# Kernel optimization log

Hardware: AMD Instinct MI355X
Metric: run time of the kernel (lower is better)

Reference implementation:

```python
import jax, jax.numpy as jnp
import numpy as np

B, S = 64, 256
VOCAB, DL, DA, DV = 30522, 300, 74, 35
DH, GH, LH, RH = 128, 64, 128, 128  # modality dim, proj-GRU hidden, LSTM hidden, RGN hidden


def _gru_dir(x, Wi, Wh, bi, bh):
    # x: [B,S,D] -> [B,S,H]; torch GRU gate order (r, z, n)
    xg = x @ Wi + bi  # [B,S,3H] precomputed input projections
    H = Wh.shape[0]
    def step(h, xg_t):
        hg = h @ Wh + bh
        xr, xz, xn = jnp.split(xg_t, 3, axis=-1)
        hr, hz, hn = jnp.split(hg, 3, axis=-1)
        r = jax.nn.sigmoid(xr + hr)
        z = jax.nn.sigmoid(xz + hz)
        n = jnp.tanh(xn + r * hn)
        h = (1.0 - z) * n + z * h
        return h, h
    h0 = jnp.zeros((x.shape[0], H), x.dtype)
    _, ys = jax.lax.scan(step, h0, jnp.swapaxes(xg, 0, 1))
    return jnp.swapaxes(ys, 0, 1)


def _bigru(x, Wi, Wh, bi, bh):
    f = _gru_dir(x, Wi[0], Wh[0], bi[0], bh[0])
    b = _gru_dir(x[:, ::-1], Wi[1], Wh[1], bi[1], bh[1])[:, ::-1]
    return jnp.concatenate([f, b], axis=-1)


def _lstm_dir(x, Wi, Wh, bi, bh):
    xg = x @ Wi + bi  # [B,S,4H]; torch LSTM gate order (i, f, g, o)
    H = Wh.shape[0]
    def step(carry, xg_t):
        h, c = carry
        g = xg_t + h @ Wh + bh
        i, f, gg, o = jnp.split(g, 4, axis=-1)
        c = jax.nn.sigmoid(f) * c + jax.nn.sigmoid(i) * jnp.tanh(gg)
        h = jax.nn.sigmoid(o) * jnp.tanh(c)
        return (h, c), h
    z = jnp.zeros((x.shape[0], H), x.dtype)
    _, ys = jax.lax.scan(step, (z, z), jnp.swapaxes(xg, 0, 1))
    return jnp.swapaxes(ys, 0, 1)


def _bilstm(x, Wi, Wh, bi, bh):
    f = _lstm_dir(x, Wi[0], Wh[0], bi[0], bh[0])
    b = _lstm_dir(x[:, ::-1], Wi[1], Wh[1], bi[1], bh[1])[:, ::-1]
    return jnp.concatenate([f, b], axis=-1)


def _rgn_scan(x, h0, Wx, Wh, b):
    # RGNCell: gated recurrent cell (GRU-style), returns final state [B,H]
    xg = x @ Wx + b  # [B,S,3H]
    def step(h, xg_t):
        hg = h @ Wh
        xr, xz, xn = jnp.split(xg_t, 3, axis=-1)
        hr, hz, hn = jnp.split(hg, 3, axis=-1)
        r = jax.nn.sigmoid(xr + hr)
        z = jax.nn.sigmoid(xz + hz)
        n = jnp.tanh(xn + r * hn)
        return (1.0 - z) * n + z * h, None
    h, _ = jax.lax.scan(step, h0, jnp.swapaxes(xg, 0, 1))
    return h


def _xattn(q, kv):
    # parameter-free scaled dot-product cross-modal attention (JCAF)
    scale = 1.0 / np.sqrt(q.shape[-1]).astype(np.float32)
    s = jnp.einsum('bsd,btd->bst', q, kv) * scale
    return jnp.einsum('bst,btd->bsd', jax.nn.softmax(s, axis=-1), kv)


def _forward(sentences, acoustic, video, state0, state1, emb,
             proj_l_W, proj_l_b, proj_a_W, proj_a_b, proj_v_W, proj_v_b,
             gru_Wi, gru_Wh, gru_bi, gru_bh,
             lstm_Wi, lstm_Wh, lstm_bi, lstm_bh,
             rgn_Wx, rgn_Wh, rgn_b, fc1_W, fc1_b, fc2_W, fc2_b):
    enc = emb[sentences]                          # LanguageEmbeddingLayer: [B,S,DL]
    # SeqEncoder: project each modality to 128-d (dropout off in eval)
    seq_l = enc @ proj_l_W + proj_l_b             # [B,S,128]
    seq_a = acoustic @ proj_a_W + proj_a_b
    seq_v = video @ proj_v_W + proj_v_b
    # project_l/a/v: bidirectional GRU 128 -> 2*64 = 128
    x_l = _bigru(seq_l, gru_Wi[0], gru_Wh[0], gru_bi[0], gru_bh[0])
    x_a = _bigru(seq_a, gru_Wi[1], gru_Wh[1], gru_bi[1], gru_bh[1])
    x_v = _bigru(seq_v, gru_Wi[2], gru_Wh[2], gru_bi[2], gru_bh[2])
    # JCAF: each modality enriched by cross-attention to the other two
    fin_txt = x_l + _xattn(x_l, x_a) + _xattn(x_l, x_v)
    fin_aud = x_a + _xattn(x_a, x_l) + _xattn(x_a, x_v)
    fin_vis = x_v + _xattn(x_v, x_l) + _xattn(x_v, x_a)
    tstep = jnp.concatenate([fin_txt, fin_aud, fin_vis], axis=-1)      # [B,S,384]
    step_fusion = _bilstm(tstep, lstm_Wi, lstm_Wh, lstm_bi, lstm_bh)   # [B,S,256]
    # two custom RGNCell recurrences: forward sweep + reversed sweep
    out0 = _rgn_scan(step_fusion, state0, rgn_Wx[0], rgn_Wh[0], rgn_b[0])
    out1 = _rgn_scan(step_fusion[:, ::-1], state1, rgn_Wx[1], rgn_Wh[1], rgn_b[1])
    h = jax.nn.leaky_relu((out0 + out1) @ fc1_W + fc1_b)
    return h @ fc2_W + fc2_b                     # [B,1]


def setup_inputs():
    keys = iter(jax.random.split(jax.random.key(0), 48))
    def rn(shape, s=0.05):
        return jax.random.normal(next(keys), shape, jnp.float32) * s
    return {
        'sentences': jax.random.randint(next(keys), (B, S), 0, VOCAB),
        'acoustic': jax.random.normal(next(keys), (B, S, DA), jnp.float32),
        'video': jax.random.normal(next(keys), (B, S, DV), jnp.float32),
        'state0': jax.random.normal(next(keys), (B, RH), jnp.float32),
        'state1': jax.random.normal(next(keys), (B, RH), jnp.float32),
        'emb': rn((VOCAB, DL), 0.1),
        'proj_l_W': rn((DL, DH)), 'proj_l_b': rn((DH,)),
        'proj_a_W': rn((DA, DH)), 'proj_a_b': rn((DH,)),
        'proj_v_W': rn((DV, DH)), 'proj_v_b': rn((DH,)),
        'gru_Wi': rn((3, 2, DH, 3 * GH)), 'gru_Wh': rn((3, 2, GH, 3 * GH)),
        'gru_bi': rn((3, 2, 3 * GH)), 'gru_bh': rn((3, 2, 3 * GH)),
        'lstm_Wi': rn((2, 3 * DH, 4 * LH)), 'lstm_Wh': rn((2, LH, 4 * LH)),
        'lstm_bi': rn((2, 4 * LH)), 'lstm_bh': rn((2, 4 * LH)),
        'rgn_Wx': rn((2, 2 * LH, 3 * RH)), 'rgn_Wh': rn((2, RH, 3 * RH)),
        'rgn_b': rn((2, 3 * RH)),
        'fc1_W': rn((RH, 32)), 'fc1_b': rn((32,)),
        'fc2_W': rn((32, 1)), 'fc2_b': rn((1,)),
    }


def reference(sentences, acoustic, video, state0, state1, emb,
              proj_l_W, proj_l_b, proj_a_W, proj_a_b, proj_v_W, proj_v_b,
              gru_Wi, gru_Wh, gru_bi, gru_bh,
              lstm_Wi, lstm_Wh, lstm_bi, lstm_bh,
              rgn_Wx, rgn_Wh, rgn_b, fc1_W, fc1_b, fc2_W, fc2_b):
    return _forward(sentences, acoustic, video, state0, state1, emb,
                    proj_l_W, proj_l_b, proj_a_W, proj_a_b, proj_v_W, proj_v_b,
                    gru_Wi, gru_Wh, gru_bi, gru_bh,
                    lstm_Wi, lstm_Wh, lstm_bi, lstm_bh,
                    rgn_Wx, rgn_Wh, rgn_b, fc1_W, fc1_b, fc2_W, fc2_b)
```

## Files before the change

### kernel.cpp

```cpp
#include <hip/hip_runtime.h>

#define WS_SEQ      0LL
#define WS_XGGRU    6291456LL
#define WS_X        0LL
#define WS_TSTEP    18874368LL
#define WS_S        6291456LL
#define WS_XGLSTM   0LL
#define WS_SF       16777216LL
#define WS_XGRGN    0LL
#define WS_OUT0     20971520LL

__device__ __forceinline__ float sigf(float x) {
    return __builtin_amdgcn_rcpf(1.f + __expf(-x));
}
__device__ __forceinline__ float tanhfast(float x) {
    float e = __expf(2.f * x);
    return 1.f - 2.f * __builtin_amdgcn_rcpf(e + 1.f);
}
__device__ __forceinline__ float rl(float v, int i) {
    return __int_as_float(__builtin_amdgcn_readlane(__float_as_int(v), i));
}

typedef float vf16 __attribute__((ext_vector_type(16)));
typedef float vf2 __attribute__((ext_vector_type(2)));

#define LD16(V, P, S) { _Pragma("unroll") \
    for (int _j = 0; _j < 16; ++_j) (V)[_j] = (P)[_j * (S)]; }
#define DOT16(ACC, V, H, B) { _Pragma("unroll") \
    for (int _j = 0; _j < 16; ++_j) (ACC) = fmaf(rl((H), (B) + _j), (V)[_j], (ACC)); }

#define LDW64(W, P, S) { _Pragma("unroll") \
    for (int _k = 0; _k < 64; ++_k) (W)[_k] = *(const vf2*)((P) + _k * (S)); }

#define PK4(A0, A1, Wa, Wb, Wc, Wd, H, K0, K1, K2, K3) \
  asm("v_readlane_b32 s60, %6, " #K0 "\n\t" \
      "v_readlane_b32 s62, %6, " #K1 "\n\t" \
      "v_readlane_b32 s64, %6, " #K2 "\n\t" \
      "v_readlane_b32 s66, %6, " #K3 "\n\t" \
      "s_mov_b32 s61, s60\n\t" \
      "s_mov_b32 s63, s62\n\t" \
      "s_mov_b32 s65, s64\n\t" \
      "s_mov_b32 s67, s66\n\t" \
      "v_pk_fma_f32 %0, %2, s[60:61], %0\n\t" \
      "v_pk_fma_f32 %1, %3, s[62:63], %1\n\t" \
      "v_pk_fma_f32 %0, %4, s[64:65], %0\n\t" \
      "v_pk_fma_f32 %1, %5, s[66:67], %1" \
      : "+v"(A0), "+v"(A1) \
      : "v"(Wa), "v"(Wb), "v"(Wc), "v"(Wd), "v"(H) \
      : "s60","s61","s62","s63","s64","s65","s66","s67");

#define PKALL(A0, A1, W, H) \
  PK4(A0,A1,W[0],W[1],W[2],W[3],H,0,1,2,3) \
  PK4(A0,A1,W[4],W[5],W[6],W[7],H,4,5,6,7) \
  PK4(A0,A1,W[8],W[9],W[10],W[11],H,8,9,10,11) \
  PK4(A0,A1,W[12],W[13],W[14],W[15],H,12,13,14,15) \
  PK4(A0,A1,W[16],W[17],W[18],W[19],H,16,17,18,19) \
  PK4(A0,A1,W[20],W[21],W[22],W[23],H,20,21,22,23) \
  PK4(A0,A1,W[24],W[25],W[26],W[27],H,24,25,26,27) \
  PK4(A0,A1,W[28],W[29],W[30],W[31],H,28,29,30,31) \
  PK4(A0,A1,W[32],W[33],W[34],W[35],H,32,33,34,35) \
  PK4(A0,A1,W[36],W[37],W[38],W[39],H,36,37,38,39) \
  PK4(A0,A1,W[40],W[41],W[42],W[43],H,40,41,42,43) \
  PK4(A0,A1,W[44],W[45],W[46],W[47],H,44,45,46,47) \
  PK4(A0,A1,W[48],W[49],W[50],W[51],H,48,49,50,51) \
  PK4(A0,A1,W[52],W[53],W[54],W[55],H,52,53,54,55) \
  PK4(A0,A1,W[56],W[57],W[58],W[59],H,56,57,58,59) \
  PK4(A0,A1,W[60],W[61],W[62],W[63],H,60,61,62,63)

__device__ __forceinline__ void gemm_body(
    const float* __restrict__ Ab, int lda, const int* __restrict__ idx,
    const float* __restrict__ Wb, int wld, int wtrans,
    const float* __restrict__ bb,
    float* __restrict__ Cb, int ldc,
    int K, float alpha, int accum)
{
    int m0 = blockIdx.y * 64, n0 = blockIdx.x * 64;
    int t = threadIdx.x;
    int tx = t & 7, ty = t >> 3;

    __shared__ __align__(16) float As[16][68];
    __shared__ __align__(16) float Ws[16][68];

    vf2 acc2[8][4];
#pragma unroll
    for (int i = 0; i < 8; ++i)
#pragma unroll
        for (int j = 0; j < 4; ++j) acc2[i][j] = (vf2){0.f, 0.f};

    long long arow[4];
#pragma unroll
    for (int i = 0; i < 4; ++i) {
        int m = (t + i * 64) >> 2;
        arow[i] = idx ? (long long)idx[m0 + m] : (long long)(m0 + m);
    }
    const bool a_vec = ((lda & 3) == 0);

    for (int k0 = 0; k0 < K; k0 += 16) {
#pragma unroll
        for (int i = 0; i < 4; ++i) {
            int j = t + i * 64;
            int m = j >> 2, kq = j & 3;
            int kk = k0 + kq * 4;
            const float* p = Ab + arow[i] * (long long)lda + kk;
            float4 v = {0.f, 0.f, 0.f, 0.f};
            if (a_vec && kk + 3 < K) {
                v = *(const float4*)p;
            } else {
                if (kk + 0 < K) v.x = p[0];
                if (kk + 1 < K) v.y = p[1];
                if (kk + 2 < K) v.z = p[2];
                if (kk + 3 < K) v.w = p[3];
            }
            As[kq * 4 + 0][m] = v.x; As[kq * 4 + 1][m] = v.y;
            As[kq * 4 + 2][m] = v.z; As[kq * 4 + 3][m] = v.w;
        }
        if (!wtrans) {
#pragma unroll
            for (int i = 0; i < 4; ++i) {
                int j = t + i * 64;
                int k = j >> 4, nq = j & 15;
                float4 v = {0.f, 0.f, 0.f, 0.f};
                if (k0 + k < K)
                    v = *(const float4*)(Wb + (long long)(k0 + k) * wld + n0 + nq * 4);
                *(float4*)&Ws[k][nq * 4] = v;
            }
        } else {
#pragma unroll
            for (int i = 0; i < 4; ++i) {
                int j = t + i * 64;
                int n = j >> 2, kq = j & 3;
                int kk = k0 + kq * 4;
                const float* p = Wb + (long long)(n0 + n) * wld + kk;
                float4 v = {0.f, 0.f, 0.f, 0.f};
                if (kk + 3 < K) v = *(const float4*)p;
                else {
                    if (kk + 0 < K) v.x = p[0];
                    if (kk + 1 < K) v.y = p[1];
                    if (kk + 2 < K) v.z = p[2];
                    if (kk + 3 < K) v.w = p[3];
                }
                Ws[kq * 4 + 0][n] = v.x; Ws[kq * 4 + 1][n] = v.y;
                Ws[kq * 4 + 2][n] = v.z; Ws[kq * 4 + 3][n] = v.w;
            }
        }
        __syncthreads();
#pragma unroll
        for (int k = 0; k < 16; ++k) {
            float4 a0 = *(const float4*)&As[k][ty * 8];
            float4 a1 = *(const float4*)&As[k][ty * 8 + 4];
            float4 b0 = *(const float4*)&Ws[k][tx * 8];
            float4 b1 = *(const float4*)&Ws[k][tx * 8 + 4];
            float av[8] = {a0.x, a0.y, a0.z, a0.w, a1.x, a1.y, a1.z, a1.w};
            vf2 bv[4];
            bv[0] = (vf2){b0.x, b0.y}; bv[1] = (vf2){b0.z, b0.w};
            bv[2] = (vf2){b1.x, b1.y}; bv[3] = (vf2){b1.z, b1.w};
#pragma unroll
            for (int i = 0; i < 8; ++i) {
                vf2 a2 = {av[i], av[i]};
#pragma unroll
                for (int j = 0; j < 4; ++j)
                    acc2[i][j] = __builtin_elementwise_fma(a2, bv[j], acc2[i][j]);
            }
        }
        __syncthreads();
    }

#pragma unroll
    for (int i = 0; i < 8; ++i) {
        long long gm = m0 + ty * 8 + i;
#pragma unroll
        for (int jq = 0; jq < 2; ++jq) {
            float* cp = Cb + gm * ldc + n0 + tx * 8 + jq * 4;
            float4 v;
            v.x = alpha * acc2[i][jq * 2 + 0][0];
            v.y = alpha * acc2[i][jq * 2 + 0][1];
            v.z = alpha * acc2[i][jq * 2 + 1][0];
            v.w = alpha * acc2[i][jq * 2 + 1][1];
            if (bb) {
                const float* bp = bb + n0 + tx * 8 + jq * 4;
                v.x += bp[0]; v.y += bp[1]; v.z += bp[2]; v.w += bp[3];
            }
            if (accum) {
                float4 o = *(const float4*)cp;
                v.x += o.x; v.y += o.y; v.z += o.z; v.w += o.w;
            }
            *(float4*)cp = v;
        }
    }
}

__global__ __launch_bounds__(64) void gemm_k(
    const float* __restrict__ A, long long a_z, int a_zdiv, int lda,
    const int* __restrict__ idx,
    const float* __restrict__ W, long long w_z, int wld, int wtrans,
    const float* __restrict__ bias, int bias_z,
    float* __restrict__ C, long long c_z, int ldc,
    int K, float alpha, int accum)
{
    int z = blockIdx.z;
    gemm_body(A + (long long)(z / a_zdiv) * a_z, lda, idx,
              W + (long long)z * w_z, wld, wtrans,
              bias ? bias + (long long)z * bias_z : nullptr,
              C + (long long)z * c_z, ldc, K, alpha, accum);
}

__global__ __launch_bounds__(64) void att_score_k(
    const float* __restrict__ X, float* __restrict__ S,
    int q0, int q1, int q2, int k0, int k1, int k2)
{
    int z = blockIdx.z;
    int pair = z >> 6, b = z & 63;
    int qi = pair == 0 ? q0 : (pair == 1 ? q1 : q2);
    int ki = pair == 0 ? k0 : (pair == 1 ? k1 : k2);
    gemm_body(X + (long long)qi * 2097152 + (long long)b * 32768, 128, nullptr,
              X + (long long)ki * 2097152 + (long long)b * 32768, 128, 1,
              nullptr,
              S + (long long)z * 65536, 256, 128, 0.08838834764831845f, 0);
}

__global__ __launch_bounds__(64) void att_apply_k(
    const float* __restrict__ S, const float* __restrict__ X,
    float* __restrict__ tstep,
    int q0, int q1, int q2, int k0, int k1, int k2)
{
    int z = blockIdx.z;
    int pair = z >> 6, b = z & 63;
    int qi = pair == 0 ? q0 : (pair == 1 ? q1 : q2);
    int ki = pair == 0 ? k0 : (pair == 1 ? k1 : k2);
    gemm_body(S + (long long)z * 65536, 256, nullptr,
              X + (long long)ki * 2097152 + (long long)b * 32768, 128, 0,
              nullptr,
              tstep + (long long)qi * 128 + (long long)b * 98304, 384,
              256, 1.f, 1);
}

__global__ __launch_bounds__(256) void copy_tstep_k(const float* __restrict__ x,
                                                    float* __restrict__ tstep)
{
    int o = blockIdx.x * 256 + threadIdx.x;
    int c = o % 384;
    int row = o / 384;
    int m = c >> 7, cc = c & 127;
    tstep[o] = x[(long long)m * 2097152 + (long long)row * 128 + cc];
}

__global__ __launch_bounds__(256) void softmax_k(float* __restrict__ S)
{
    int wave = threadIdx.x >> 6, lane = threadIdx.x & 63;
    int row = blockIdx.x * 4 + wave;
    float* p = S + (long long)row * 256;
    float v[4];
    float mx = -1e30f;
#pragma unroll
    for (int i = 0; i < 4; ++i) { v[i] = p[lane + i * 64]; mx = fmaxf(mx, v[i]); }
#pragma unroll
    for (int off = 32; off > 0; off >>= 1) mx = fmaxf(mx, __shfl_xor(mx, off));
    float sum = 0.f;
#pragma unroll
    for (int i = 0; i < 4; ++i) { v[i] = __expf(v[i] - mx); sum += v[i]; }
#pragma unroll
    for (int off = 32; off > 0; off >>= 1) sum += __shfl_xor(sum, off);
    float inv = 1.f / sum;
#pragma unroll
    for (int i = 0; i < 4; ++i) p[lane + i * 64] = v[i] * inv;
}

__global__ __launch_bounds__(192) void gru_rec_k(const float* __restrict__ xg,
                                                 const float* __restrict__ Wh,
                                                 const float* __restrict__ bh,
                                                 float* __restrict__ xout)
{
    int b = blockIdx.x, z = blockIdx.y;
    int m = z >> 1, d = z & 1;
    int tid = threadIdx.x, lane = tid & 63;
    int c = tid;
    const float* Whz = Wh + (long long)z * 12288;
    const float* wp = Whz + c;
    vf16 W0, W1, W2, W3;
    LD16(W0, wp + 0 * 16 * 192, 192); LD16(W1, wp + 1 * 16 * 192, 192);
    LD16(W2, wp + 2 * 16 * 192, 192); LD16(W3, wp + 3 * 16 * 192, 192);
    float bias = bh[z * 192 + c];

    __shared__ float g[2][192];
    int n = lane;
    float h = 0.f;
    const float* xgb = xg + (long long)z * 3145728 + (long long)b * 49152;
    float* xob = xout + (long long)m * 2097152 + (long long)b * 32768 + d * 64;
    int tt0 = d ? 255 : 0;
    const float* xr0 = xgb + tt0 * 192;
    float x_r = xr0[n], x_z = xr0[64 + n], x_n = xr0[128 + n];

#pragma unroll 1
    for (int t = 0; t < 256; ++t) {
        int tt = d ? 255 - t : t;
        float nx_r = 0, nx_z = 0, nx_n = 0;
        if (t < 255) {
            const float* xr = xgb + (d ? tt - 1 : tt + 1) * 192;
            nx_r = xr[n]; nx_z = xr[64 + n]; nx_n = xr[128 + n];
        }
        float s0 = bias, s1 = 0.f, s2 = 0.f, s3 = 0.f;
        DOT16(s0, W0, h, 0);  DOT16(s1, W1, h, 16);
        DOT16(s2, W2, h, 32); DOT16(s3, W3, h, 48);
        g[t & 1][c] = (s0 + s1) + (s2 + s3);
        __syncthreads();
        const float* gp = g[t & 1];
        float r  = sigf(x_r + gp[n]);
        float zz = sigf(x_z + gp[64 + n]);
        float nn = tanhfast(x_n + r * gp[128 + n]);
        h = (1.f - zz) * nn + zz * h;
        if (c < 64) xob[tt * 128 + n] = h;
        x_r = nx_r; x_z = nx_z; x_n = nx_n;
    }
}

__global__ __launch_bounds__(512) void lstm_rec_k(const float* __restrict__ xg,
                                                  const float* __restrict__ Wh,
                                                  const float* __restrict__ bh,
                                                  float* __restrict__ sf)
{
    int b = blockIdx.x, d = blockIdx.y;
    int tid = threadIdx.x, lane = tid & 63;
    int kh = tid >> 8;
    int cp = tid & 255;
    const float* Whz = Wh + (long long)d * 65536;
    const float* wp = Whz + (long long)(kh * 64) * 512 + 2 * cp;
    vf2 Wk[64];
    LDW64(Wk, wp, 512);

    __shared__ float part[2][1024];
    int n = kh * 64 + lane;
    float h = 0.f, cst = 0.f;
    const float* xgb = xg + (long long)d * 8388608 + (long long)b * 131072;
    float* sfb = sf + (long long)b * 65536 + d * 128;

    vf2 bias2 = {0.f, 0.f}, xc2 = {0.f, 0.f};
    if (kh == 0) {
        bias2 = *(const vf2*)(bh + d * 512 + 2 * cp);
        int tt0 = d ? 255 : 0;
        xc2 = *(const vf2*)(xgb + tt0 * 512 + 2 * cp);
    }

#pragma unroll 1
    for (int t = 0; t < 256; ++t) {
        int tt = d ? 255 - t : t;
        vf2 nxc2 = {0.f, 0.f};
        if (kh == 0 && t < 255)
            nxc2 = *(const vf2*)(xgb + (d ? tt - 1 : tt + 1) * 512 + 2 * cp);
        vf2 a0 = xc2 + bias2, a1 = {0.f, 0.f};
        PKALL(a0, a1, Wk, h);
        *(vf2*)&part[t & 1][kh * 512 + 2 * cp] = a0 + a1;
        __syncthreads();
        const float* p = part[t & 1];
        float iv = p[n]       + p[512 + n];
        float fv = p[128 + n] + p[512 + 128 + n];
        float gv = p[256 + n] + p[512 + 256 + n];
        float ov = p[384 + n] + p[512 + 384 + n];
        cst = sigf(fv) * cst + sigf(iv) * tanhfast(gv);
        h = sigf(ov) * tanhfast(cst);
        if (cp < 64) sfb[tt * 256 + n] = h;
        xc2 = nxc2;
    }
}

__global__ __launch_bounds__(768) void rgn_rec_k(const float* __restrict__ xg,
                                                 const float* __restrict__ Wh,
                                                 const float* __restrict__ state0,
                                                 const float* __restrict__ state1,
                                                 float* __restrict__ outbase)
{
    int b = blockIdx.x, d = blockIdx.y;
    int tid = threadIdx.x, lane = tid & 63;
    int kh = (tid >= 384) ? 1 : 0;
    int c  = tid - kh * 384;
    const float* Whz = Wh + (long long)d * 49152;
    const float* wp = Whz + (long long)(kh * 64) * 384 + c;
    vf16 W0, W1, W2, W3;
    LD16(W0, wp + 0 * 16 * 384, 384); LD16(W1, wp + 1 * 16 * 384, 384);
    LD16(W2, wp + 2 * 16 * 384, 384); LD16(W3, wp + 3 * 16 * 384, 384);

    __shared__ float part[2][768];
    int n = kh * 64 + lane;
    const float* st = d ? state1 : state0;
    float h = st[b * 128 + n];
    const float* xgb = xg + (long long)d * 6291456 + (long long)b * 98304;
    int tt0 = d ? 255 : 0;
    const float* xr0 = xgb + tt0 * 384;
    float x_r = xr0[n], x_z = xr0[128 + n], x_n = xr0[256 + n];

#pragma unroll 1
    for (int t = 0; t < 256; ++t) {
        int tt = d ? 255 - t : t;
        float nx_r = 0, nx_z = 0, nx_n = 0;
        if (t < 255) {
            const float* xr = xgb + (d ? tt - 1 : tt + 1) * 384;
            nx_r = xr[n]; nx_z = xr[128 + n]; nx_n = xr[256 + n];
        }
        float s0 = 0.f, s1 = 0.f, s2 = 0.f, s3 = 0.f;
        DOT16(s0, W0, h, 0);  DOT16(s1, W1, h, 16);
        DOT16(s2, W2, h, 32); DOT16(s3, W3, h, 48);
        part[t & 1][kh * 384 + c] = (s0 + s1) + (s2 + s3);
        __syncthreads();
        const float* p = part[t & 1];
        float pr = p[n]       + p[384 + n];
        float pz = p[128 + n] + p[384 + 128 + n];
        float pn = p[256 + n] + p[384 + 256 + n];
        float r  = sigf(x_r + pr);
        float zz = sigf(x_z + pz);
        float nn = tanhfast(x_n + r * pn);
        h = (1.f - zz) * nn + zz * h;
        x_r = nx_r; x_z = nx_z; x_n = nx_n;
    }
    if (c < 64) outbase[(long long)d * 8192 + b * 128 + n] = h;
}

__global__ __launch_bounds__(256) void fc_k(const float* __restrict__ o01,
                                            const float* __restrict__ f1W,
                                            const float* __restrict__ f1b,
                                            const float* __restrict__ f2W,
                                            const float* __restrict__ f2b,
                                            float* __restrict__ out)
{
    __shared__ float s[8192];
    __shared__ float h1[2048];
    int tid = threadIdx.x;
    for (int e = tid; e < 8192; e += 256) s[e] = o01[e] + o01[8192 + e];
    __syncthreads();
    for (int o = tid; o < 2048; o += 256) {
        int b = o >> 5, q = o & 31;
        float acc = f1b[q];
        for (int k = 0; k < 128; ++k) acc += s[b * 128 + k] * f1W[k * 32 + q];
        h1[o] = acc >= 0.f ? acc : 0.01f * acc;
    }
    __syncthreads();
    if (tid < 64) {
        float acc = f2b[0];
        for (int q = 0; q < 32; ++q) acc += h1[tid * 32 + q] * f2W[q];
        out[tid] = acc;
    }
}

extern "C" void kernel_launch(void* const* d_in, const int* in_sizes, int n_in,
                              void* d_out, int out_size, void* d_ws, size_t ws_size,
                              hipStream_t stream)
{
    const int*   sent     = (const int*)  d_in[0];
    const float* acoustic = (const float*)d_in[1];
    const float* video    = (const float*)d_in[2];
    const float* state0   = (const float*)d_in[3];
    const float* state1   = (const float*)d_in[4];
    const float* emb      = (const float*)d_in[5];
    const float* plW = (const float*)d_in[6],  *plb = (const float*)d_in[7];
    const float* paW = (const float*)d_in[8],  *pab = (const float*)d_in[9];
    const float* pvW = (const float*)d_in[10], *pvb = (const float*)d_in[11];
    const float* gWi = (const float*)d_in[12], *gWh = (const float*)d_in[13];
    const float* gbi = (const float*)d_in[14], *gbh = (const float*)d_in[15];
    const float* lWi = (const float*)d_in[16], *lWh = (const float*)d_in[17];
    const float* lbi = (const float*)d_in[18], *lbh = (const float*)d_in[19];
    const float* rWx = (const float*)d_in[20], *rWh = (const float*)d_in[21];
    const float* rb  = (const float*)d_in[22];
    const float* f1W = (const float*)d_in[23], *f1b = (const float*)d_in[24];
    const float* f2W = (const float*)d_in[25], *f2b = (const float*)d_in[26];
    float* ws  = (float*)d_ws;
    float* out = (float*)d_out;

    dim3 blk(64);

    gemm_k<<<dim3(2, 256, 1), blk, 0, stream>>>(emb, 0, 1, 300, sent,
        plW, 0, 128, 0, plb, 0, ws + WS_SEQ, 0, 128, 300, 1.f, 0);
    gemm_k<<<dim3(2, 256, 1), blk, 0, stream>>>(acoustic, 0, 1, 74, nullptr,
        paW, 0, 128, 0, pab, 0, ws + WS_SEQ + 2097152, 0, 128, 74, 1.f, 0);
    gemm_k<<<dim3(2, 256, 1), blk, 0, stream>>>(video, 0, 1, 35, nullptr,
        pvW, 0, 128, 0, pvb, 0, ws + WS_SEQ + 4194304, 0, 128, 35, 1.f, 0);

    gemm_k<<<dim3(3, 256, 6), blk, 0, stream>>>(ws + WS_SEQ, 2097152, 2, 128, nullptr,
        gWi, 24576, 192, 0, gbi, 192, ws + WS_XGGRU, 3145728, 192, 128, 1.f, 0);

    gru_rec_k<<<dim3(64, 6), dim3(192), 0, stream>>>(ws + WS_XGGRU, gWh, gbh, ws + WS_X);

    copy_tstep_k<<<dim3(24576), dim3(256), 0, stream>>>(ws + WS_X, ws + WS_TSTEP);

    att_score_k<<<dim3(4, 4, 192), blk, 0, stream>>>(ws + WS_X, ws + WS_S,
        0, 1, 2, 1, 0, 0);
    softmax_k<<<dim3(12288), dim3(256), 0, stream>>>(ws + WS_S);
    att_apply_k<<<dim3(2, 4, 192), blk, 0, stream>>>(ws + WS_S, ws + WS_X,
        ws + WS_TSTEP, 0, 1, 2, 1, 0, 0);
    att_score_k<<<dim3(4, 4, 192), blk, 0, stream>>>(ws + WS_X, ws + WS_S,
        0, 1, 2, 2, 2, 1);
    softmax_k<<<dim3(12288), dim3(256), 0, stream>>>(ws + WS_S);
    att_apply_k<<<dim3(2, 4, 192), blk, 0, stream>>>(ws + WS_S, ws + WS_X,
        ws + WS_TSTEP, 0, 1, 2, 2, 2, 1);

    gemm_k<<<dim3(8, 256, 2), blk, 0, stream>>>(ws + WS_TSTEP, 0, 1, 384, nullptr,
        lWi, 196608, 512, 0, lbi, 512, ws + WS_XGLSTM, 8388608, 512, 384, 1.f, 0);

    lstm_rec_k<<<dim3(64, 2), dim3(512), 0, stream>>>(ws + WS_XGLSTM, lWh, lbh, ws + WS_SF);

    gemm_k<<<dim3(6, 256, 2), blk, 0, stream>>>(ws + WS_SF, 0, 1, 256, nullptr,
        rWx, 98304, 384, 0, rb, 384, ws + WS_XGRGN, 6291456, 384, 256, 1.f, 0);

    rgn_rec_k<<<dim3(64, 2), dim3(768), 0, stream>>>(ws + WS_XGRGN, rWh, state0, state1,
                                                     ws + WS_OUT0);

    fc_k<<<dim3(1), dim3(256), 0, stream>>>(ws + WS_OUT0, f1W, f1b, f2W, f2b, out);
}
```

Baseline: 1.579 ms.

## Move recurrent weights from registers into LDS and halve RGN block size

The GRU, LSTM and RGN recurrence kernels no longer hold recurrent weight slices in VGPRs. The GRU keeps the whole Wh in shared memory. LSTM and RGN put most rows in LDS (144 KB) and read the rest from global/L2 on every step. RGN now uses 384 threads, each computing two output columns with packed FMA. The goal is to lower register pressure and block size, at the cost of an LDS or global read inside the serial per-step dot product.

```diff
diff --git a/kernel.cpp b/kernel.cpp
--- a/kernel.cpp
+++ b/kernel.cpp
@@ -21,51 +21,7 @@
     return __int_as_float(__builtin_amdgcn_readlane(__float_as_int(v), i));
 }
 
-typedef float vf16 __attribute__((ext_vector_type(16)));
 typedef float vf2 __attribute__((ext_vector_type(2)));
-
-#define LD16(V, P, S) { _Pragma("unroll") \
-    for (int _j = 0; _j < 16; ++_j) (V)[_j] = (P)[_j * (S)]; }
-#define DOT16(ACC, V, H, B) { _Pragma("unroll") \
-    for (int _j = 0; _j < 16; ++_j) (ACC) = fmaf(rl((H), (B) + _j), (V)[_j], (ACC)); }
-
-#define LDW64(W, P, S) { _Pragma("unroll") \
-    for (int _k = 0; _k < 64; ++_k) (W)[_k] = *(const vf2*)((P) + _k * (S)); }
-
-#define PK4(A0, A1, Wa, Wb, Wc, Wd, H, K0, K1, K2, K3) \
-  asm("v_readlane_b32 s60, %6, " #K0 "\n\t" \
-      "v_readlane_b32 s62, %6, " #K1 "\n\t" \
-      "v_readlane_b32 s64, %6, " #K2 "\n\t" \
-      "v_readlane_b32 s66, %6, " #K3 "\n\t" \
-      "s_mov_b32 s61, s60\n\t" \
-      "s_mov_b32 s63, s62\n\t" \
-      "s_mov_b32 s65, s64\n\t" \
-      "s_mov_b32 s67, s66\n\t" \
-      "v_pk_fma_f32 %0, %2, s[60:61], %0\n\t" \
-      "v_pk_fma_f32 %1, %3, s[62:63], %1\n\t" \
-      "v_pk_fma_f32 %0, %4, s[64:65], %0\n\t" \
-      "v_pk_fma_f32 %1, %5, s[66:67], %1" \
-      : "+v"(A0), "+v"(A1) \
-      : "v"(Wa), "v"(Wb), "v"(Wc), "v"(Wd), "v"(H) \
-      : "s60","s61","s62","s63","s64","s65","s66","s67");
-
-#define PKALL(A0, A1, W, H) \
-  PK4(A0,A1,W[0],W[1],W[2],W[3],H,0,1,2,3) \
-  PK4(A0,A1,W[4],W[5],W[6],W[7],H,4,5,6,7) \
-  PK4(A0,A1,W[8],W[9],W[10],W[11],H,8,9,10,11) \
-  PK4(A0,A1,W[12],W[13],W[14],W[15],H,12,13,14,15) \
-  PK4(A0,A1,W[16],W[17],W[18],W[19],H,16,17,18,19) \
-  PK4(A0,A1,W[20],W[21],W[22],W[23],H,20,21,22,23) \
-  PK4(A0,A1,W[24],W[25],W[26],W[27],H,24,25,26,27) \
-  PK4(A0,A1,W[28],W[29],W[30],W[31],H,28,29,30,31) \
-  PK4(A0,A1,W[32],W[33],W[34],W[35],H,32,33,34,35) \
-  PK4(A0,A1,W[36],W[37],W[38],W[39],H,36,37,38,39) \
-  PK4(A0,A1,W[40],W[41],W[42],W[43],H,40,41,42,43) \
-  PK4(A0,A1,W[44],W[45],W[46],W[47],H,44,45,46,47) \
-  PK4(A0,A1,W[48],W[49],W[50],W[51],H,48,49,50,51) \
-  PK4(A0,A1,W[52],W[53],W[54],W[55],H,52,53,54,55) \
-  PK4(A0,A1,W[56],W[57],W[58],W[59],H,56,57,58,59) \
-  PK4(A0,A1,W[60],W[61],W[62],W[63],H,60,61,62,63)
 
 __device__ __forceinline__ void gemm_body(
     const float* __restrict__ Ab, int lda, const int* __restrict__ idx,
@@ -275,13 +231,12 @@
     int tid = threadIdx.x, lane = tid & 63;
     int c = tid;
     const float* Whz = Wh + (long long)z * 12288;
-    const float* wp = Whz + c;
-    vf16 W0, W1, W2, W3;
-    LD16(W0, wp + 0 * 16 * 192, 192); LD16(W1, wp + 1 * 16 * 192, 192);
-    LD16(W2, wp + 2 * 16 * 192, 192); LD16(W3, wp + 3 * 16 * 192, 192);
+    __shared__ __align__(16) float wlds[12288];
+    __shared__ float g[2][192];
+    for (int i = tid; i < 3072; i += 192)
+        ((float4*)wlds)[i] = ((const float4*)Whz)[i];
     float bias = bh[z * 192 + c];
 
-    __shared__ float g[2][192];
     int n = lane;
     float h = 0.f;
     const float* xgb = xg + (long long)z * 3145728 + (long long)b * 49152;
@@ -289,6 +244,7 @@
     int tt0 = d ? 255 : 0;
     const float* xr0 = xgb + tt0 * 192;
     float x_r = xr0[n], x_z = xr0[64 + n], x_n = xr0[128 + n];
+    __syncthreads();
 
 #pragma unroll 1
     for (int t = 0; t < 256; ++t) {
@@ -299,8 +255,13 @@
             nx_r = xr[n]; nx_z = xr[64 + n]; nx_n = xr[128 + n];
         }
         float s0 = bias, s1 = 0.f, s2 = 0.f, s3 = 0.f;
-        DOT16(s0, W0, h, 0);  DOT16(s1, W1, h, 16);
-        DOT16(s2, W2, h, 32); DOT16(s3, W3, h, 48);
+#pragma unroll
+        for (int j = 0; j < 16; ++j) {
+            s0 = fmaf(rl(h, j),      wlds[j * 192 + c],        s0);
+            s1 = fmaf(rl(h, 16 + j), wlds[(16 + j) * 192 + c], s1);
+            s2 = fmaf(rl(h, 32 + j), wlds[(32 + j) * 192 + c], s2);
+            s3 = fmaf(rl(h, 48 + j), wlds[(48 + j) * 192 + c], s3);
+        }
         g[t & 1][c] = (s0 + s1) + (s2 + s3);
         __syncthreads();
         const float* gp = g[t & 1];
@@ -323,11 +284,17 @@
     int kh = tid >> 8;
     int cp = tid & 255;
     const float* Whz = Wh + (long long)d * 65536;
-    const float* wp = Whz + (long long)(kh * 64) * 512 + 2 * cp;
-    vf2 Wk[64];
-    LDW64(Wk, wp, 512);
-
+
+    __shared__ __align__(16) float wlds[36864];
     __shared__ float part[2][1024];
+    for (int i = tid; i < 9216; i += 512) {
+        int row = i >> 7, c4 = (i & 127) << 2;
+        int srow = row < 36 ? row : row + 28;
+        *(float4*)&wlds[row * 512 + c4] = *(const float4*)(Whz + srow * 512 + c4);
+    }
+    const float* wl  = wlds + (kh * 36) * 512 + 2 * cp;
+    const float* wpg = Whz + (long long)(kh * 64 + 36) * 512 + 2 * cp;
+
     int n = kh * 64 + lane;
     float h = 0.f, cst = 0.f;
     const float* xgb = xg + (long long)d * 8388608 + (long long)b * 131072;
@@ -339,6 +306,7 @@
         int tt0 = d ? 255 : 0;
         xc2 = *(const vf2*)(xgb + tt0 * 512 + 2 * cp);
     }
+    __syncthreads();
 
 #pragma unroll 1
     for (int t = 0; t < 256; ++t) {
@@ -347,7 +315,22 @@
         if (kh == 0 && t < 255)
             nxc2 = *(const vf2*)(xgb + (d ? tt - 1 : tt + 1) * 512 + 2 * cp);
         vf2 a0 = xc2 + bias2, a1 = {0.f, 0.f};
-        PKALL(a0, a1, Wk, h);
+#pragma unroll
+        for (int r = 0; r < 36; ++r) {
+            float hs = rl(h, r);
+            vf2 hb = {hs, hs};
+            vf2 w = *(const vf2*)(wl + r * 512);
+            if (r & 1) a1 = __builtin_elementwise_fma(hb, w, a1);
+            else       a0 = __builtin_elementwise_fma(hb, w, a0);
+        }
+#pragma unroll
+        for (int r = 0; r < 28; ++r) {
+            float hs = rl(h, 36 + r);
+            vf2 hb = {hs, hs};
+            vf2 w = *(const vf2*)(wpg + r * 512);
+            if (r & 1) a1 = __builtin_elementwise_fma(hb, w, a1);
+            else       a0 = __builtin_elementwise_fma(hb, w, a0);
+        }
         *(vf2*)&part[t & 1][kh * 512 + 2 * cp] = a0 + a1;
         __syncthreads();
         const float* p = part[t & 1];
@@ -362,7 +345,7 @@
     }
 }
 
-__global__ __launch_bounds__(768) void rgn_rec_k(const float* __restrict__ xg,
+__global__ __launch_bounds__(384) void rgn_rec_k(const float* __restrict__ xg,
                                                  const float* __restrict__ Wh,
                                                  const float* __restrict__ state0,
                                                  const float* __restrict__ state1,
@@ -370,15 +353,20 @@
 {
     int b = blockIdx.x, d = blockIdx.y;
     int tid = threadIdx.x, lane = tid & 63;
-    int kh = (tid >= 384) ? 1 : 0;
-    int c  = tid - kh * 384;
+    int kh = (tid >= 192) ? 1 : 0;
+    int cp = tid - kh * 192;
     const float* Whz = Wh + (long long)d * 49152;
-    const float* wp = Whz + (long long)(kh * 64) * 384 + c;
-    vf16 W0, W1, W2, W3;
-    LD16(W0, wp + 0 * 16 * 384, 384); LD16(W1, wp + 1 * 16 * 384, 384);
-    LD16(W2, wp + 2 * 16 * 384, 384); LD16(W3, wp + 3 * 16 * 384, 384);
-
+
+    __shared__ __align__(16) float wlds[36864];
     __shared__ float part[2][768];
+    for (int i = tid; i < 9216; i += 384) {
+        int row = i / 96, c4 = (i % 96) << 2;
+        int srow = row < 48 ? row : row + 16;
+        *(float4*)&wlds[row * 384 + c4] = *(const float4*)(Whz + srow * 384 + c4);
+    }
+    const float* wl  = wlds + (kh * 48) * 384 + 2 * cp;
+    const float* wpg = Whz + (long long)(kh * 64 + 48) * 384 + 2 * cp;
+
     int n = kh * 64 + lane;
     const float* st = d ? state1 : state0;
     float h = st[b * 128 + n];
@@ -386,6 +374,7 @@
     int tt0 = d ? 255 : 0;
     const float* xr0 = xgb + tt0 * 384;
     float x_r = xr0[n], x_z = xr0[128 + n], x_n = xr0[256 + n];
+    __syncthreads();
 
 #pragma unroll 1
     for (int t = 0; t < 256; ++t) {
@@ -395,10 +384,24 @@
             const float* xr = xgb + (d ? tt - 1 : tt + 1) * 384;
             nx_r = xr[n]; nx_z = xr[128 + n]; nx_n = xr[256 + n];
         }
-        float s0 = 0.f, s1 = 0.f, s2 = 0.f, s3 = 0.f;
-        DOT16(s0, W0, h, 0);  DOT16(s1, W1, h, 16);
-        DOT16(s2, W2, h, 32); DOT16(s3, W3, h, 48);
-        part[t & 1][kh * 384 + c] = (s0 + s1) + (s2 + s3);
+        vf2 a0 = {0.f, 0.f}, a1 = {0.f, 0.f};
+#pragma unroll
+        for (int r = 0; r < 48; ++r) {
+            float hs = rl(h, r);
+            vf2 hb = {hs, hs};
+            vf2 w = *(const vf2*)(wl + r * 384);
+            if (r & 1) a1 = __builtin_elementwise_fma(hb, w, a1);
+            else       a0 = __builtin_elementwise_fma(hb, w, a0);
+        }
+#pragma unroll
+        for (int r = 0; r < 16; ++r) {
+            float hs = rl(h, 48 + r);
+            vf2 hb = {hs, hs};
+            vf2 w = *(const vf2*)(wpg + r * 384);
+            if (r & 1) a1 = __builtin_elementwise_fma(hb, w, a1);
+            else       a0 = __builtin_elementwise_fma(hb, w, a0);
+        }
+        *(vf2*)&part[t & 1][kh * 384 + 2 * cp] = a0 + a1;
         __syncthreads();
         const float* p = part[t & 1];
         float pr = p[n]       + p[384 + n];
@@ -410,7 +413,7 @@
         h = (1.f - zz) * nn + zz * h;
         x_r = nx_r; x_z = nx_z; x_n = nx_n;
     }
-    if (c < 64) outbase[(long long)d * 8192 + b * 128 + n] = h;
+    if (cp < 64) outbase[(long long)d * 8192 + b * 128 + n] = h;
 }
 
 __global__ __launch_bounds__(256) void fc_k(const float* __restrict__ o01,
@@ -498,7 +501,7 @@
     gemm_k<<<dim3(6, 256, 2), blk, 0, stream>>>(ws + WS_SF, 0, 1, 256, nullptr,
         rWx, 98304, 384, 0, rb, 384, ws + WS_XGRGN, 6291456, 384, 256, 1.f, 0);
 
-    rgn_rec_k<<<dim3(64, 2), dim3(768), 0, stream>>>(ws + WS_XGRGN, rWh, state0, state1,
+    rgn_rec_k<<<dim3(64, 2), dim3(384), 0, stream>>>(ws + WS_XGRGN, rWh, state0, state1,
                                                      ws + WS_OUT0);
 
     fc_k<<<dim3(1), dim3(256), 0, stream>>>(ws + WS_OUT0, f1W, f1b, f2W, f2b, out);
```

Result: slower. 1.754 ms (+11.1%).
